# Kernel optimization log

Hardware: AMD Instinct MI355X
Metric: run time of the kernel (lower is better)

The kernel has to match this reference:

```python
import jax, jax.numpy as jnp
import numpy as np

CHUNK = 64
NORM_EPS = 1e-5
DENOM_EPS = 1.0
B, S, HID, H = 4, 4096, 1024, 8
D = HID // H  # 128


def rmsnorm(x, w, eps=NORM_EPS):
    var = jnp.mean(x * x, axis=-1, keepdims=True)
    return x * jax.lax.rsqrt(var + eps) * w


def chunked_linear_attn(q, k, v):
    # q,k,v: [B,S,H,D]; causal linear attention o_s = q_s @ sum_{t<=s} k_t^T v_t
    b, s, h, d = q.shape
    n = s // CHUNK
    def to_chunks(x):
        return x.reshape(b, n, CHUNK, h, d).transpose(1, 0, 3, 2, 4)  # [N,B,H,C,D]
    qc, kc, vc = to_chunks(q), to_chunks(k), to_chunks(v)
    mask = jnp.tril(jnp.ones((CHUNK, CHUNK), dtype=q.dtype))
    def step(state, inp):
        qq, kk, vv = inp  # [B,H,C,D]
        inter = jnp.einsum('bhcd,bhde->bhce', qq, state)
        scores = jnp.einsum('bhcd,bhed->bhce', qq, kk) * mask  # causal intra-chunk
        intra = jnp.einsum('bhce,bhed->bhcd', scores, vv)
        state = state + jnp.einsum('bhcd,bhce->bhde', kk, vv)
        return state, inter + intra
    init = jnp.zeros((b, h, d, d), dtype=q.dtype)
    _, o = jax.lax.scan(step, init, (qc, kc, vc))  # [N,B,H,C,D]
    return o.transpose(1, 0, 3, 2, 4).reshape(b, s, h, d)


def setup_inputs() -> dict:
    key = jax.random.key(0)
    k0, k1, k2, k3, k4 = jax.random.split(key, 5)
    hidden_states = jax.random.normal(k0, (B, S, HID), dtype=jnp.float32)
    Wq = jax.random.normal(k1, (HID, HID), dtype=jnp.float32) * 0.02
    Wk = jax.random.normal(k2, (HID, HID), dtype=jnp.float32) * 0.02
    Wv = jax.random.normal(k3, (HID, HID), dtype=jnp.float32) * 0.02
    Wo = jax.random.normal(k4, (HID, HID), dtype=jnp.float32) * 0.02
    norm_w = jnp.ones((D,), dtype=jnp.float32)
    return {"hidden_states": hidden_states, "Wq": Wq, "Wk": Wk, "Wv": Wv, "Wo": Wo, "norm_w": norm_w}


def reference(hidden_states, Wq, Wk, Wv, Wo, norm_w):
    b, s, _ = hidden_states.shape
    q = jnp.einsum('bsd,ed->bse', hidden_states, Wq).reshape(b, s, H, D)
    k = jnp.einsum('bsd,ed->bse', hidden_states, Wk).reshape(b, s, H, D)
    v = jnp.einsum('bsd,ed->bse', hidden_states, Wv).reshape(b, s, H, D)
    # feature_map='identity', norm_q/norm_k=False
    o = chunked_linear_attn(q, k, v)  # [B,S,H,D]
    z = jnp.cumsum(k, axis=1)
    denom = jnp.maximum(jnp.abs(jnp.sum(q * z, axis=-1)), DENOM_EPS)[..., None]
    o = o / denom
    o = rmsnorm(o, norm_w)
    o = o.reshape(b, s, H * D)
    return jnp.einsum('bse,de->bsd', o, Wo)
```

## Files before the change

kernel.cpp:

```cpp
#include <hip/hip_runtime.h>
#include <stdint.h>

typedef __bf16 bf16x8 __attribute__((ext_vector_type(8)));
typedef float  f32x4  __attribute__((ext_vector_type(4)));

static __device__ __forceinline__ void gload16(const void* g, void* l) {
  __builtin_amdgcn_global_load_lds((__attribute__((address_space(1))) void*)g,
                                   (__attribute__((address_space(3))) void*)l,
                                   16, 0, 0);
}

static __device__ __forceinline__ f32x4 mfma16(bf16x8 a, bf16x8 b, f32x4 c) {
  return __builtin_amdgcn_mfma_f32_16x16x32_bf16(a, b, c, 0, 0, 0);
}

#define MEMFENCE asm volatile("" ::: "memory")

__global__ __launch_bounds__(256) void cast8_k(const float* __restrict__ in,
                                               __bf16* __restrict__ out) {
  const size_t i = ((size_t)blockIdx.x * 256 + threadIdx.x) * 8;
  const float4 v0 = *(const float4*)(in + i);
  const float4 v1 = *(const float4*)(in + i + 4);
  bf16x8 o;
  o[0] = (__bf16)v0.x; o[1] = (__bf16)v0.y; o[2] = (__bf16)v0.z; o[3] = (__bf16)v0.w;
  o[4] = (__bf16)v1.x; o[5] = (__bf16)v1.y; o[6] = (__bf16)v1.z; o[7] = (__bf16)v1.w;
  *(bf16x8*)(out + i) = o;
}

__global__ __launch_bounds__(256) void castw_k(const float* __restrict__ w0, const float* __restrict__ w1,
                                               const float* __restrict__ w2, const float* __restrict__ w3,
                                               __bf16* __restrict__ o0, __bf16* __restrict__ o1,
                                               __bf16* __restrict__ o2, __bf16* __restrict__ o3) {
  const float* in; __bf16* out;
  switch (blockIdx.y) {
    case 0: in = w0; out = o0; break;
    case 1: in = w1; out = o1; break;
    case 2: in = w2; out = o2; break;
    default: in = w3; out = o3; break;
  }
  const size_t i = ((size_t)blockIdx.x * 256 + threadIdx.x) * 8;
  const float4 v0 = *(const float4*)(in + i);
  const float4 v1 = *(const float4*)(in + i + 4);
  bf16x8 o;
  o[0] = (__bf16)v0.x; o[1] = (__bf16)v0.y; o[2] = (__bf16)v0.z; o[3] = (__bf16)v0.w;
  o[4] = (__bf16)v1.x; o[5] = (__bf16)v1.y; o[6] = (__bf16)v1.z; o[7] = (__bf16)v1.w;
  *(bf16x8*)(out + i) = o;
}

static __device__ __forceinline__ void kloop256(
    const __bf16* __restrict__ A, const __bf16* __restrict__ W,
    int m0, int n0, __bf16* sh, int tid, f32x4 acc[8][4]) {
  const int l = tid & 63;
  const int wv = tid >> 6;
  const int wm = wv >> 2, wn = wv & 3;
  const int lo = l & 15, kq = l >> 4;

  auto SA = [&](int kt, int h) {
#pragma unroll
    for (int j = 0; j < 2; ++j) {
      const int p = j * 512 + tid;
      const int r = p >> 3, sl = p & 7;
      const int grow = m0 + h * 64 + (r & 63) + (r >> 6) * 128;
      gload16(A + (size_t)grow * 1024 + (kt << 6) + ((sl ^ (r & 7)) << 3),
              sh + (kt & 1) * 32768 + h * 8192 + p * 8);
    }
  };
  auto SB = [&](int kt, int h) {
#pragma unroll
    for (int j = 0; j < 2; ++j) {
      const int p = j * 512 + tid;
      const int r = p >> 3, sl = p & 7;
      const int grow = n0 + h * 32 + (r & 31) + (r >> 5) * 64;
      gload16(W + (size_t)grow * 1024 + (kt << 6) + ((sl ^ (r & 7)) << 3),
              sh + (kt & 1) * 32768 + 16384 + h * 8192 + p * 8);
    }
  };
  auto LDA = [&](int cur, int mh, int mi, int ks) -> bf16x8 {
    const int r = wm * 64 + mi * 16 + lo;
    return *(const bf16x8*)&sh[cur * 32768 + mh * 8192 + r * 64 + (((ks * 4 + kq) ^ (r & 7)) << 3)];
  };
  auto LDB = [&](int cur, int nh, int ni, int ks) -> bf16x8 {
    const int r = wn * 32 + ni * 16 + lo;
    return *(const bf16x8*)&sh[cur * 32768 + 16384 + nh * 8192 + r * 64 + (((ks * 4 + kq) ^ (r & 7)) << 3)];
  };

  SA(0, 0); SB(0, 0); SB(0, 1); SA(0, 1);
  SA(1, 0); SB(1, 1); SA(1, 1);
  MEMFENCE;
  asm volatile("s_waitcnt vmcnt(6)" ::: "memory");
  __builtin_amdgcn_s_barrier();

  bf16x8 a[4][2], b[2][2], b2[2][2];
#pragma unroll 2
  for (int t = 0; t < 16; ++t) {
    const int cur = t & 1;
#pragma unroll
    for (int mi = 0; mi < 4; ++mi)
#pragma unroll
      for (int ks = 0; ks < 2; ++ks) a[mi][ks] = LDA(cur, 0, mi, ks);
#pragma unroll
    for (int ni = 0; ni < 2; ++ni)
#pragma unroll
      for (int ks = 0; ks < 2; ++ks) b[ni][ks] = LDB(cur, 0, ni, ks);
    if (t + 1 < 16) SB(t + 1, 0);
    MEMFENCE;
    asm volatile("s_waitcnt lgkmcnt(0)" ::: "memory");
    __builtin_amdgcn_sched_barrier(0);
    __builtin_amdgcn_s_setprio(1);
#pragma unroll
    for (int mi = 0; mi < 4; ++mi)
#pragma unroll
      for (int ni = 0; ni < 2; ++ni)
#pragma unroll
        for (int ks = 0; ks < 2; ++ks)
          acc[mi][ni] = mfma16(a[mi][ks], b[ni][ks], acc[mi][ni]);
    __builtin_amdgcn_s_setprio(0);
    MEMFENCE;
    __builtin_amdgcn_s_barrier();
#pragma unroll
    for (int ni = 0; ni < 2; ++ni)
#pragma unroll
      for (int ks = 0; ks < 2; ++ks) b2[ni][ks] = LDB(cur, 1, ni, ks);
    if (t + 2 < 16) SA(t + 2, 0);
    MEMFENCE;
    asm volatile("s_waitcnt lgkmcnt(0)" ::: "memory");
    __builtin_amdgcn_sched_barrier(0);
    __builtin_amdgcn_s_setprio(1);
#pragma unroll
    for (int mi = 0; mi < 4; ++mi)
#pragma unroll
      for (int ni = 0; ni < 2; ++ni)
#pragma unroll
        for (int ks = 0; ks < 2; ++ks)
          acc[mi][2 + ni] = mfma16(a[mi][ks], b2[ni][ks], acc[mi][2 + ni]);
    __builtin_amdgcn_s_setprio(0);
    MEMFENCE;
    __builtin_amdgcn_s_barrier();
#pragma unroll
    for (int mi = 0; mi < 4; ++mi)
#pragma unroll
      for (int ks = 0; ks < 2; ++ks) a[mi][ks] = LDA(cur, 1, mi, ks);
    if (t + 2 < 16) SB(t + 2, 1);
    MEMFENCE;
    asm volatile("s_waitcnt lgkmcnt(0)" ::: "memory");
    __builtin_amdgcn_sched_barrier(0);
    __builtin_amdgcn_s_setprio(1);
#pragma unroll
    for (int mi = 0; mi < 4; ++mi)
#pragma unroll
      for (int ni = 0; ni < 2; ++ni)
#pragma unroll
        for (int ks = 0; ks < 2; ++ks)
          acc[4 + mi][2 + ni] = mfma16(a[mi][ks], b2[ni][ks], acc[4 + mi][2 + ni]);
    __builtin_amdgcn_s_setprio(0);
    MEMFENCE;
    __builtin_amdgcn_s_barrier();
#pragma unroll
    for (int ni = 0; ni < 2; ++ni)
#pragma unroll
      for (int ks = 0; ks < 2; ++ks) b[ni][ks] = LDB(cur, 0, ni, ks);
    if (t + 2 < 16) SA(t + 2, 1);
    MEMFENCE;
    asm volatile("s_waitcnt lgkmcnt(0)" ::: "memory");
    __builtin_amdgcn_sched_barrier(0);
    __builtin_amdgcn_s_setprio(1);
#pragma unroll
    for (int mi = 0; mi < 4; ++mi)
#pragma unroll
      for (int ni = 0; ni < 2; ++ni)
#pragma unroll
        for (int ks = 0; ks < 2; ++ks)
          acc[4 + mi][ni] = mfma16(a[mi][ks], b[ni][ks], acc[4 + mi][ni]);
    __builtin_amdgcn_s_setprio(0);
    if (t < 14) asm volatile("s_waitcnt vmcnt(6)" ::: "memory");
    else        asm volatile("s_waitcnt vmcnt(0)" ::: "memory");
    MEMFENCE;
    __builtin_amdgcn_s_barrier();
  }
}

__global__ __launch_bounds__(512, 2)
void gemm_qkv8_k(const __bf16* __restrict__ A,
                 const __bf16* __restrict__ Bq, const __bf16* __restrict__ Bk, const __bf16* __restrict__ Bv,
                 __bf16* __restrict__ Qo, __bf16* __restrict__ Ko,
                 __bf16* __restrict__ Kt, __bf16* __restrict__ Vt) {
  extern __shared__ __bf16 sh[];
  const int tid = threadIdx.x;
  const int flat = blockIdx.x;
  const int sf = (flat & 7) * 96 + (flat >> 3);
  const int z = sf >> 8;
  const int rem = sf & 255;
  const int m0 = (rem >> 2) * 256;
  const int n0 = (rem & 3) * 256;
  const __bf16* W = (z == 0) ? Bq : (z == 1) ? Bk : Bv;

  f32x4 acc[8][4] = {};
  kloop256(A, W, m0, n0, sh, tid, acc);

  const int l = tid & 63, wv = tid >> 6, wm = wv >> 2, wn = wv & 3;
  const int lo = l & 15, kq = l >> 4;

  if (z <= 1) {
    __bf16* R = z ? Ko : Qo;
#pragma unroll
    for (int nh = 0; nh < 2; ++nh) {
      if ((wn >> 1) == nh) {
#pragma unroll
        for (int mi = 0; mi < 8; ++mi)
#pragma unroll
          for (int ni = 0; ni < 4; ++ni)
#pragma unroll
            for (int rr = 0; rr < 4; ++rr)
              sh[wm * 17408 + (mi * 16 + kq * 4 + rr) * 136 + (wn & 1) * 64 + ni * 16 + lo]
                  = (__bf16)acc[mi][ni][rr];
      }
      __syncthreads();
#pragma unroll
      for (int it = 0; it < 8; ++it) {
        const int idx = it * 512 + tid;
        const int rg = idx >> 11, mrow = (idx >> 4) & 127, sl = idx & 15;
        *(bf16x8*)(R + (size_t)(m0 + rg * 128 + mrow) * 1024 + n0 + nh * 128 + sl * 8)
            = *(const bf16x8*)&sh[rg * 17408 + mrow * 136 + sl * 8];
      }
      __syncthreads();
    }
  }
  if (z >= 1) {
    __bf16* T = (z == 1) ? Kt : Vt;
    const int bb = m0 >> 12, s0v = m0 & 4095, h0 = n0 >> 7;
#pragma unroll
    for (int nh = 0; nh < 2; ++nh) {
      if ((wn >> 1) == nh) {
#pragma unroll
        for (int mi = 0; mi < 8; ++mi)
#pragma unroll
          for (int ni = 0; ni < 4; ++ni)
#pragma unroll
            for (int rr = 0; rr < 4; ++rr)
              sh[wm * 17408 + ((wn & 1) * 64 + ni * 16 + lo) * 136 + mi * 16 + kq * 4 + rr]
                  = (__bf16)acc[mi][ni][rr];
      }
      __syncthreads();
      const int hh = h0 + nh;
#pragma unroll
      for (int it = 0; it < 8; ++it) {
        const int idx = it * 512 + tid;
        const int rg = idx >> 11, dr = (idx >> 4) & 127, sl = idx & 15;
        *(bf16x8*)(T + ((size_t)((bb * 8 + hh) * 128 + dr)) * 4096 + s0v + rg * 128 + sl * 8)
            = *(const bf16x8*)&sh[rg * 17408 + dr * 136 + sl * 8];
      }
      __syncthreads();
    }
  }
}

__global__ __launch_bounds__(512, 2)
void gemm_out8_k(const __bf16* __restrict__ A, const __bf16* __restrict__ W,
                 float* __restrict__ Co) {
  extern __shared__ __bf16 sh[];
  const int tid = threadIdx.x;
  const int flat = blockIdx.x;
  const int sf = (flat & 7) * 32 + (flat >> 3);
  const int m0 = (sf >> 2) * 256;
  const int n0 = (sf & 3) * 256;

  f32x4 acc[8][4] = {};
  kloop256(A, W, m0, n0, sh, tid, acc);

  const int l = tid & 63, wv = tid >> 6, wm = wv >> 2, wn = wv & 3;
  const int lo = l & 15, kq = l >> 4;
#pragma unroll
  for (int mi = 0; mi < 8; ++mi)
#pragma unroll
    for (int ni = 0; ni < 4; ++ni)
#pragma unroll
      for (int rr = 0; rr < 4; ++rr)
        Co[(size_t)(m0 + wm * 128 + mi * 16 + kq * 4 + rr) * 1024 + n0 + wn * 64 + ni * 16 + lo]
            = acc[mi][ni][rr];
}

__global__ __launch_bounds__(128)
void z2_k(float* __restrict__ zc) {
  const int bh = blockIdx.x;
  const int d = threadIdx.x;
  float run = 0.0f;
  for (int cc = 0; cc < 64; ++cc) {
    float* p = zc + (size_t)(bh * 64 + cc) * 128 + d;
    const float old = *p;
    *p = run;
    run += old;
  }
}

__global__ __launch_bounds__(256)
void passA_k(const __bf16* __restrict__ Kt, const __bf16* __restrict__ Vt,
             __bf16* __restrict__ Sc, float* __restrict__ zc) {
  const int c = blockIdx.x, bh = blockIdx.y;
  const int tid = threadIdx.x, l = tid & 63, w = tid >> 6;
  const int wr = (w >> 1) * 64, wc = (w & 1) * 64;
  const int lr = l & 15, lk = (l >> 4) * 8;
  f32x4 acc[4][4] = {};
  float zac[4] = {0.0f, 0.0f, 0.0f, 0.0f};
#pragma unroll
  for (int kk = 0; kk < 2; ++kk) {
    const int t = c * 64 + kk * 32 + lk;
    bf16x8 av[4], bk[4];
#pragma unroll
    for (int mt = 0; mt < 4; ++mt)
      av[mt] = *(const bf16x8*)(Vt + ((size_t)(bh * 128 + wr + mt * 16 + lr)) * 4096 + t);
#pragma unroll
    for (int nt = 0; nt < 4; ++nt) {
      bk[nt] = *(const bf16x8*)(Kt + ((size_t)(bh * 128 + wc + nt * 16 + lr)) * 4096 + t);
#pragma unroll
      for (int e = 0; e < 8; ++e) zac[nt] += (float)bk[nt][e];
    }
#pragma unroll
    for (int mt = 0; mt < 4; ++mt)
#pragma unroll
      for (int nt = 0; nt < 4; ++nt)
        acc[mt][nt] = mfma16(av[mt], bk[nt], acc[mt][nt]);
  }
#pragma unroll
  for (int nt = 0; nt < 4; ++nt) {
    zac[nt] += __shfl_xor(zac[nt], 16);
    zac[nt] += __shfl_xor(zac[nt], 32);
  }
  if (w < 2 && l < 16) {
#pragma unroll
    for (int nt = 0; nt < 4; ++nt)
      zc[(size_t)(bh * 64 + c) * 128 + wc + nt * 16 + lr] = zac[nt];
  }
  const size_t sbase = ((size_t)(bh * 64 + c)) << 14;
#pragma unroll
  for (int mt = 0; mt < 4; ++mt)
#pragma unroll
    for (int r = 0; r < 4; ++r) {
      const int e = wr + mt * 16 + (l >> 4) * 4 + r;
#pragma unroll
      for (int nt = 0; nt < 4; ++nt) {
        const int d = wc + nt * 16 + lr;
        Sc[sbase + (size_t)e * 128 + d] = (__bf16)acc[mt][nt][r];
      }
    }
}

__global__ __launch_bounds__(256)
void passB_k(__bf16* __restrict__ Sc) {
  const int bh = blockIdx.y;
  const int idx = blockIdx.x * 256 + threadIdx.x;
  float run = 0.0f;
  for (int cc = 0; cc < 64; ++cc) {
    __bf16* p = Sc + (((size_t)(bh * 64 + cc)) << 14) + idx;
    const float old = (float)*p;
    *p = (__bf16)run;
    run += old;
  }
}

__global__ __launch_bounds__(256)
void passC_k(const __bf16* __restrict__ Q, const __bf16* __restrict__ K,
             const __bf16* __restrict__ Vt, const __bf16* __restrict__ Sp,
             const float* __restrict__ zp, const float* __restrict__ nw,
             __bf16* __restrict__ O) {
  alignas(16) __shared__ __bf16 ScL[64 * 72];
  alignas(16) __shared__ float OL[64 * 132];
  alignas(16) __shared__ float zPL[128];
  alignas(16) __shared__ float nwL[128];
  alignas(16) __shared__ float dnL[64];
  const int c = blockIdx.x, bh = blockIdx.y;
  const int bb = bh >> 3, hh = bh & 7;
  const int tid = threadIdx.x, l = tid & 63, wv = tid >> 6;
  const int lr = l & 15, lk = (l >> 4) * 8;
  if (tid < 128) zPL[tid] = zp[(size_t)(bh * 64 + c) * 128 + tid];
  else nwL[tid - 128] = nw[tid - 128];

  const size_t qbase = ((size_t)(bb * 4096 + c * 64)) * 1024 + hh * 128;
  const size_t sbase = ((size_t)(bh * 64 + c)) << 14;

  f32x4 accO[4][2] = {};
  f32x4 accS[4] = {};
#pragma unroll
  for (int kk = 0; kk < 4; ++kk) {
    const int dof = kk * 32 + lk;
    bf16x8 aQ[4], bS[2], bK;
#pragma unroll
    for (int mt = 0; mt < 4; ++mt)
      aQ[mt] = *(const bf16x8*)(Q + qbase + (size_t)(mt * 16 + lr) * 1024 + dof);
#pragma unroll
    for (int nt = 0; nt < 2; ++nt)
      bS[nt] = *(const bf16x8*)(Sp + sbase + (size_t)(wv * 32 + nt * 16 + lr) * 128 + dof);
    bK = *(const bf16x8*)(K + qbase + (size_t)(wv * 16 + lr) * 1024 + dof);
#pragma unroll
    for (int mt = 0; mt < 4; ++mt) {
      accS[mt] = mfma16(aQ[mt], bK, accS[mt]);
#pragma unroll
      for (int nt = 0; nt < 2; ++nt)
        accO[mt][nt] = mfma16(aQ[mt], bS[nt], accO[mt][nt]);
    }
  }
#pragma unroll
  for (int mt = 0; mt < 4; ++mt)
#pragma unroll
    for (int r = 0; r < 4; ++r) {
      const int srow = mt * 16 + (l >> 4) * 4 + r;
      const int tcol = wv * 16 + lr;
      ScL[srow * 72 + tcol] = (__bf16)((tcol <= srow) ? accS[mt][r] : 0.0f);
    }
  __syncthreads();
#pragma unroll
  for (int kk2 = 0; kk2 < 2; ++kk2) {
    const int tof = kk2 * 32 + lk;
    bf16x8 aS[4], bV[2];
#pragma unroll
    for (int mt = 0; mt < 4; ++mt) aS[mt] = *(const bf16x8*)&ScL[(mt * 16 + lr) * 72 + tof];
#pragma unroll
    for (int nt = 0; nt < 2; ++nt)
      bV[nt] = *(const bf16x8*)(Vt + ((size_t)(bh * 128 + wv * 32 + nt * 16 + lr)) * 4096 + c * 64 + tof);
#pragma unroll
    for (int mt = 0; mt < 4; ++mt)
#pragma unroll
      for (int nt = 0; nt < 2; ++nt)
        accO[mt][nt] = mfma16(aS[mt], bV[nt], accO[mt][nt]);
  }
  {
    const int s = tid >> 2, grp = tid & 3;
    float rs = 0.0f;
#pragma unroll
    for (int t = 0; t < 16; ++t) rs += (float)ScL[s * 72 + grp * 16 + t];
    float qz = 0.0f;
    const __bf16* qrow = Q + qbase + (size_t)s * 1024 + grp * 32;
#pragma unroll
    for (int j = 0; j < 4; ++j) {
      const bf16x8 q8 = *(const bf16x8*)(qrow + j * 8);
#pragma unroll
      for (int i = 0; i < 8; ++i) qz += (float)q8[i] * zPL[grp * 32 + j * 8 + i];
    }
    float v = rs + qz;
    v += __shfl_xor(v, 1);
    v += __shfl_xor(v, 2);
    if (grp == 0) dnL[s] = fmaxf(fabsf(v), 1.0f);
  }
  __syncthreads();
#pragma unroll
  for (int mt = 0; mt < 4; ++mt)
#pragma unroll
    for (int r = 0; r < 4; ++r) {
      const int row = mt * 16 + (l >> 4) * 4 + r;
#pragma unroll
      for (int nt = 0; nt < 2; ++nt) {
        const int col = wv * 32 + nt * 16 + lr;
        OL[row * 132 + col] = accO[mt][nt][r] / dnL[row];
      }
    }
  __syncthreads();
  const int s = tid >> 2, e0 = (tid & 3) * 32;
  float ss = 0.0f;
  for (int i = 0; i < 32; ++i) { const float v = OL[s * 132 + e0 + i]; ss += v * v; }
  ss += __shfl_xor(ss, 1);
  ss += __shfl_xor(ss, 2);
  const float scale = rsqrtf(ss * (1.0f / 128.0f) + 1e-5f);
  __bf16* orow = O + qbase + (size_t)s * 1024 + e0;
#pragma unroll
  for (int i8 = 0; i8 < 4; ++i8) {
    bf16x8 ov;
#pragma unroll
    for (int j = 0; j < 8; ++j) {
      const int e = e0 + i8 * 8 + j;
      ov[j] = (__bf16)(OL[s * 132 + e] * scale * nwL[e]);
    }
    *(bf16x8*)(orow + i8 * 8) = ov;
  }
}

extern "C" void kernel_launch(void* const* d_in, const int* in_sizes, int n_in,
                              void* d_out, int out_size, void* d_ws, size_t ws_size,
                              hipStream_t stream) {
  (void)in_sizes; (void)n_in; (void)out_size; (void)ws_size;
  const float* hid = (const float*)d_in[0];
  const float* Wq  = (const float*)d_in[1];
  const float* Wk  = (const float*)d_in[2];
  const float* Wv  = (const float*)d_in[3];
  const float* Wo  = (const float*)d_in[4];
  const float* nw  = (const float*)d_in[5];

  char* ws = (char*)d_ws;
  size_t off = 0;
  auto nxt = [&](size_t bytes) -> char* {
    char* p = ws + off;
    off += (bytes + 255) & ~(size_t)255;
    return p;
  };
  __bf16* hA  = (__bf16*)nxt(33554432);
  __bf16* wqB = (__bf16*)nxt(2097152);
  __bf16* wkB = (__bf16*)nxt(2097152);
  __bf16* wvB = (__bf16*)nxt(2097152);
  __bf16* woB = (__bf16*)nxt(2097152);
  __bf16* Qb  = (__bf16*)nxt(33554432);
  __bf16* Kb  = (__bf16*)nxt(33554432);
  __bf16* Ktb = (__bf16*)nxt(33554432);
  __bf16* Vtb = (__bf16*)nxt(33554432);
  __bf16* Scb = (__bf16*)nxt(67108864);
  float*  zcb = (float*)nxt(1048576);
  __bf16* Ob  = hA;

  cast8_k<<<8192, 256, 0, stream>>>(hid, hA);
  castw_k<<<dim3(512, 4), 256, 0, stream>>>(Wq, Wk, Wv, Wo, wqB, wkB, wvB, woB);
  gemm_qkv8_k<<<768, 512, 131072, stream>>>(hA, wqB, wkB, wvB, Qb, Kb, Ktb, Vtb);
  passA_k<<<dim3(64, 32), 256, 0, stream>>>(Ktb, Vtb, Scb, zcb);
  passB_k<<<dim3(64, 32), 256, 0, stream>>>(Scb);
  z2_k<<<32, 128, 0, stream>>>(zcb);
  passC_k<<<dim3(64, 32), 256, 0, stream>>>(Qb, Kb, Vtb, Scb, zcb, nw, Ob);
  gemm_out8_k<<<256, 512, 131072, stream>>>(Ob, woB, (float*)d_out);
}
```

Baseline: 368.1 us.

## Merge cast and prefix-scan launches and restructure GEMM k-loop into two phases

```diff
diff --git a/kernel.cpp b/kernel.cpp
--- a/kernel.cpp
+++ b/kernel.cpp
@@ -16,29 +16,26 @@
 
 #define MEMFENCE asm volatile("" ::: "memory")
 
-__global__ __launch_bounds__(256) void cast8_k(const float* __restrict__ in,
-                                               __bf16* __restrict__ out) {
-  const size_t i = ((size_t)blockIdx.x * 256 + threadIdx.x) * 8;
-  const float4 v0 = *(const float4*)(in + i);
-  const float4 v1 = *(const float4*)(in + i + 4);
-  bf16x8 o;
-  o[0] = (__bf16)v0.x; o[1] = (__bf16)v0.y; o[2] = (__bf16)v0.z; o[3] = (__bf16)v0.w;
-  o[4] = (__bf16)v1.x; o[5] = (__bf16)v1.y; o[6] = (__bf16)v1.z; o[7] = (__bf16)v1.w;
-  *(bf16x8*)(out + i) = o;
-}
-
-__global__ __launch_bounds__(256) void castw_k(const float* __restrict__ w0, const float* __restrict__ w1,
-                                               const float* __restrict__ w2, const float* __restrict__ w3,
-                                               __bf16* __restrict__ o0, __bf16* __restrict__ o1,
-                                               __bf16* __restrict__ o2, __bf16* __restrict__ o3) {
-  const float* in; __bf16* out;
-  switch (blockIdx.y) {
-    case 0: in = w0; out = o0; break;
-    case 1: in = w1; out = o1; break;
-    case 2: in = w2; out = o2; break;
-    default: in = w3; out = o3; break;
-  }
-  const size_t i = ((size_t)blockIdx.x * 256 + threadIdx.x) * 8;
+__global__ __launch_bounds__(256)
+void castall_k(const float* __restrict__ hid, const float* __restrict__ w0,
+               const float* __restrict__ w1, const float* __restrict__ w2,
+               const float* __restrict__ w3, __bf16* __restrict__ ho,
+               __bf16* __restrict__ o0, __bf16* __restrict__ o1,
+               __bf16* __restrict__ o2, __bf16* __restrict__ o3) {
+  const int bx = blockIdx.x;
+  const float* in; __bf16* out; size_t base;
+  if (bx < 8192) { in = hid; out = ho; base = (size_t)bx * 2048; }
+  else {
+    const int w = (bx - 8192) >> 9, loc = (bx - 8192) & 511;
+    switch (w) {
+      case 0: in = w0; out = o0; break;
+      case 1: in = w1; out = o1; break;
+      case 2: in = w2; out = o2; break;
+      default: in = w3; out = o3; break;
+    }
+    base = (size_t)loc * 2048;
+  }
+  const size_t i = base + (size_t)threadIdx.x * 8;
   const float4 v0 = *(const float4*)(in + i);
   const float4 v1 = *(const float4*)(in + i + 4);
   bf16x8 o;
@@ -101,76 +98,47 @@
 #pragma unroll
     for (int ni = 0; ni < 2; ++ni)
 #pragma unroll
-      for (int ks = 0; ks < 2; ++ks) b[ni][ks] = LDB(cur, 0, ni, ks);
-    if (t + 1 < 16) SB(t + 1, 0);
+      for (int ks = 0; ks < 2; ++ks) { b[ni][ks] = LDB(cur, 0, ni, ks); b2[ni][ks] = LDB(cur, 1, ni, ks); }
     MEMFENCE;
     asm volatile("s_waitcnt lgkmcnt(0)" ::: "memory");
     __builtin_amdgcn_sched_barrier(0);
+    if (t + 1 < 16) SB(t + 1, 0);
+    if (t + 2 < 16) SA(t + 2, 0);
+    MEMFENCE;
     __builtin_amdgcn_s_setprio(1);
 #pragma unroll
     for (int mi = 0; mi < 4; ++mi)
 #pragma unroll
-      for (int ni = 0; ni < 2; ++ni)
-#pragma unroll
-        for (int ks = 0; ks < 2; ++ks)
-          acc[mi][ni] = mfma16(a[mi][ks], b[ni][ks], acc[mi][ni]);
+      for (int ks = 0; ks < 2; ++ks) {
+#pragma unroll
+        for (int ni = 0; ni < 2; ++ni) {
+          acc[mi][ni]     = mfma16(a[mi][ks], b[ni][ks],  acc[mi][ni]);
+          acc[mi][2 + ni] = mfma16(a[mi][ks], b2[ni][ks], acc[mi][2 + ni]);
+        }
+      }
     __builtin_amdgcn_s_setprio(0);
     MEMFENCE;
     __builtin_amdgcn_s_barrier();
 #pragma unroll
-    for (int ni = 0; ni < 2; ++ni)
-#pragma unroll
-      for (int ks = 0; ks < 2; ++ks) b2[ni][ks] = LDB(cur, 1, ni, ks);
-    if (t + 2 < 16) SA(t + 2, 0);
+    for (int mi = 0; mi < 4; ++mi)
+#pragma unroll
+      for (int ks = 0; ks < 2; ++ks) a[mi][ks] = LDA(cur, 1, mi, ks);
     MEMFENCE;
     asm volatile("s_waitcnt lgkmcnt(0)" ::: "memory");
     __builtin_amdgcn_sched_barrier(0);
+    if (t + 2 < 16) { SB(t + 2, 1); SA(t + 2, 1); }
+    MEMFENCE;
     __builtin_amdgcn_s_setprio(1);
 #pragma unroll
     for (int mi = 0; mi < 4; ++mi)
 #pragma unroll
-      for (int ni = 0; ni < 2; ++ni)
-#pragma unroll
-        for (int ks = 0; ks < 2; ++ks)
-          acc[mi][2 + ni] = mfma16(a[mi][ks], b2[ni][ks], acc[mi][2 + ni]);
-    __builtin_amdgcn_s_setprio(0);
-    MEMFENCE;
-    __builtin_amdgcn_s_barrier();
-#pragma unroll
-    for (int mi = 0; mi < 4; ++mi)
-#pragma unroll
-      for (int ks = 0; ks < 2; ++ks) a[mi][ks] = LDA(cur, 1, mi, ks);
-    if (t + 2 < 16) SB(t + 2, 1);
-    MEMFENCE;
-    asm volatile("s_waitcnt lgkmcnt(0)" ::: "memory");
-    __builtin_amdgcn_sched_barrier(0);
-    __builtin_amdgcn_s_setprio(1);
-#pragma unroll
-    for (int mi = 0; mi < 4; ++mi)
-#pragma unroll
-      for (int ni = 0; ni < 2; ++ni)
-#pragma unroll
-        for (int ks = 0; ks < 2; ++ks)
+      for (int ks = 0; ks < 2; ++ks) {
+#pragma unroll
+        for (int ni = 0; ni < 2; ++ni) {
+          acc[4 + mi][ni]     = mfma16(a[mi][ks], b[ni][ks],  acc[4 + mi][ni]);
           acc[4 + mi][2 + ni] = mfma16(a[mi][ks], b2[ni][ks], acc[4 + mi][2 + ni]);
-    __builtin_amdgcn_s_setprio(0);
-    MEMFENCE;
-    __builtin_amdgcn_s_barrier();
-#pragma unroll
-    for (int ni = 0; ni < 2; ++ni)
-#pragma unroll
-      for (int ks = 0; ks < 2; ++ks) b[ni][ks] = LDB(cur, 0, ni, ks);
-    if (t + 2 < 16) SA(t + 2, 1);
-    MEMFENCE;
-    asm volatile("s_waitcnt lgkmcnt(0)" ::: "memory");
-    __builtin_amdgcn_sched_barrier(0);
-    __builtin_amdgcn_s_setprio(1);
-#pragma unroll
-    for (int mi = 0; mi < 4; ++mi)
-#pragma unroll
-      for (int ni = 0; ni < 2; ++ni)
-#pragma unroll
-        for (int ks = 0; ks < 2; ++ks)
-          acc[4 + mi][ni] = mfma16(a[mi][ks], b[ni][ks], acc[4 + mi][ni]);
+        }
+      }
     __builtin_amdgcn_s_setprio(0);
     if (t < 14) asm volatile("s_waitcnt vmcnt(6)" ::: "memory");
     else        asm volatile("s_waitcnt vmcnt(0)" ::: "memory");
@@ -279,19 +247,6 @@
             = acc[mi][ni][rr];
 }
 
-__global__ __launch_bounds__(128)
-void z2_k(float* __restrict__ zc) {
-  const int bh = blockIdx.x;
-  const int d = threadIdx.x;
-  float run = 0.0f;
-  for (int cc = 0; cc < 64; ++cc) {
-    float* p = zc + (size_t)(bh * 64 + cc) * 128 + d;
-    const float old = *p;
-    *p = run;
-    run += old;
-  }
-}
-
 __global__ __launch_bounds__(256)
 void passA_k(const __bf16* __restrict__ Kt, const __bf16* __restrict__ Vt,
              __bf16* __restrict__ Sc, float* __restrict__ zc) {
@@ -345,8 +300,21 @@
 }
 
 __global__ __launch_bounds__(256)
-void passB_k(__bf16* __restrict__ Sc) {
+void passBz_k(__bf16* __restrict__ Sc, float* __restrict__ zc) {
   const int bh = blockIdx.y;
+  if (blockIdx.x == 64) {
+    const int d = threadIdx.x;
+    if (d < 128) {
+      float run = 0.0f;
+      for (int cc = 0; cc < 64; ++cc) {
+        float* p = zc + (size_t)(bh * 64 + cc) * 128 + d;
+        const float old = *p;
+        *p = run;
+        run += old;
+      }
+    }
+    return;
+  }
   const int idx = blockIdx.x * 256 + threadIdx.x;
   float run = 0.0f;
   for (int cc = 0; cc < 64; ++cc) {
@@ -503,12 +471,10 @@
   float*  zcb = (float*)nxt(1048576);
   __bf16* Ob  = hA;
 
-  cast8_k<<<8192, 256, 0, stream>>>(hid, hA);
-  castw_k<<<dim3(512, 4), 256, 0, stream>>>(Wq, Wk, Wv, Wo, wqB, wkB, wvB, woB);
+  castall_k<<<10240, 256, 0, stream>>>(hid, Wq, Wk, Wv, Wo, hA, wqB, wkB, wvB, woB);
   gemm_qkv8_k<<<768, 512, 131072, stream>>>(hA, wqB, wkB, wvB, Qb, Kb, Ktb, Vtb);
   passA_k<<<dim3(64, 32), 256, 0, stream>>>(Ktb, Vtb, Scb, zcb);
-  passB_k<<<dim3(64, 32), 256, 0, stream>>>(Scb);
-  z2_k<<<32, 128, 0, stream>>>(zcb);
+  passBz_k<<<dim3(65, 32), 256, 0, stream>>>(Scb, zcb);
   passC_k<<<dim3(64, 32), 256, 0, stream>>>(Qb, Kb, Vtb, Scb, zcb, nw, Ob);
   gemm_out8_k<<<256, 512, 131072, stream>>>(Ob, woB, (float*)d_out);
 }
```

Measured after the change: 449.1 us. +22.0%, slower.
